# Kernel tuning notes

Measured on AMD Instinct MI355X. Metric: run time of the kernel, lower is better.

The kernel has to match this reference:

```python
import jax, jax.numpy as jnp
import numpy as np

B, N, F_IN, F, C, E = 8192, 68, 2, 128, 16, 272
EPS = 1e-15


def graph_conv(x, src, dst, W_rel, W_root, b):
    # PyG GraphConv (aggr='add'): out_i = W_rel @ sum_{j->i} x_j + W_root @ x_i + b
    agg = jnp.zeros(x.shape, x.dtype).at[:, dst].add(x[:, src])  # [B,N,Fin]
    return agg @ W_rel.T + x @ W_root.T + b


def setup_inputs() -> dict:
    key = jax.random.key(0)
    ks = jax.random.split(key, 12)
    x = jax.random.normal(ks[0], (B, N, F_IN), jnp.float32)
    edge_index = jax.random.randint(ks[1], (2, E), 0, N, jnp.int32)
    adj = jax.random.uniform(ks[2], (B, N, N), jnp.float32)
    s = jax.random.normal(ks[3], (B, N, C), jnp.float32)
    pos = jax.random.normal(ks[4], (B, N, F_IN), jnp.float32)
    sc = 0.1
    W1_rel = jax.random.normal(ks[5], (F, F_IN), jnp.float32) * sc
    W1_root = jax.random.normal(ks[6], (F, F_IN), jnp.float32) * sc
    b1 = jnp.zeros((F,), jnp.float32)
    W2_rel = jax.random.normal(ks[7], (F, F), jnp.float32) * sc
    W2_root = jax.random.normal(ks[8], (F, F), jnp.float32) * sc
    b2 = jnp.zeros((F,), jnp.float32)
    W3_rel = jax.random.normal(ks[9], (F, F), jnp.float32) * sc
    W3_root = jax.random.normal(ks[10], (F, F), jnp.float32) * sc
    b3 = jnp.zeros((F,), jnp.float32)
    return dict(x=x, edge_index=edge_index, adj=adj, s=s, pos=pos,
                W1_rel=W1_rel, W1_root=W1_root, b1=b1,
                W2_rel=W2_rel, W2_root=W2_root, b2=b2,
                W3_rel=W3_rel, W3_root=W3_root, b3=b3)


def reference(x, edge_index, adj, s, pos,
              W1_rel, W1_root, b1, W2_rel, W2_root, b2, W3_rel, W3_root, b3):
    src, dst = edge_index[0], edge_index[1]
    h = jax.nn.relu(graph_conv(x, src, dst, W1_rel, W1_root, b1))
    h = jax.nn.relu(graph_conv(h, src, dst, W2_rel, W2_root, b2))
    h = jax.nn.relu(graph_conv(h, src, dst, W3_rel, W3_root, b3))  # [B,N,F]
    # dense_diff_pool
    s_sm = jax.nn.softmax(s, axis=-1)                       # [B,N,C]
    out = jnp.einsum('bnc,bnf->bcf', s_sm, h)               # [B,C,F]
    out_adj = jnp.einsum('bnc,bnm,bmk->bck', s_sm, adj, s_sm)  # [B,C,C]
    diff = adj - jnp.einsum('bnc,bmc->bnm', s_sm, s_sm)
    link_loss = jnp.sqrt(jnp.sum(diff * diff)) / adj.size
    ent_loss = jnp.mean(jnp.sum(-s_sm * jnp.log(s_sm + EPS), axis=-1))
    return (out, out_adj, link_loss, ent_loss, pos)
```

## Files before the change

### kernel.cpp

```cpp
#include <hip/hip_runtime.h>
#include <math.h>

#define B_   8192
#define N_   68
#define FIN  2
#define F_   128
#define C_   16
#define E_   272

#define OUT_OFF  0
#define ADJ_OFF  (B_*C_*F_)
#define LINK_IDX (ADJ_OFF + B_*C_*C_)
#define ENT_IDX  (LINK_IDX + 1)
#define POS_OFF  (ENT_IDX + 1)

#define WS_CSR_OFF  131072
#define WS_W_OFF    133120
#define WS_AG_OFF   264192

typedef __attribute__((ext_vector_type(8))) short bf16x8;
typedef __attribute__((ext_vector_type(4))) float f32x4;

#define SWZ256(r, cb) (((r) * 256) + ((cb) ^ (((r) & 7) << 4)))
#define SWZ512(r, cb) (((r) * 512) + ((cb) ^ (((r) & 7) << 4)))
#define SWZH(r, cb)   (((r) * 192) + ((cb) ^ (((r) & 3) << 4)))
#define MFMA16(a, bb, c) __builtin_amdgcn_mfma_f32_16x16x32_bf16((a), (bb), (c), 0, 0, 0)

__device__ __forceinline__ short bf16_rne(float x) {
  unsigned u = __builtin_bit_cast(unsigned, x);
  u += 0x7FFFu + ((u >> 16) & 1u);
  return (short)(u >> 16);
}
__device__ __forceinline__ short4 pack4(f32x4 v) {
  short4 s;
  s.x = bf16_rne(v[0]); s.y = bf16_rne(v[1]); s.z = bf16_rne(v[2]); s.w = bf16_rne(v[3]);
  return s;
}

__global__ void prep_kernel(const int* __restrict__ edge_index,
                            const float* __restrict__ W2r, const float* __restrict__ W2o,
                            const float* __restrict__ W3r, const float* __restrict__ W3o,
                            int* __restrict__ csr, short* __restrict__ wcat,
                            short* __restrict__ agw) {
  int gid = blockIdx.x * blockDim.x + threadIdx.x;
  for (int e = gid; e < 2 * F_ * 256; e += gridDim.x * blockDim.x) {
    int layer = e >> 15, idx = e & 32767;
    int j = idx >> 8, k = idx & 255;
    const float* Wr = layer ? W3r : W2r;
    const float* Wo = layer ? W3o : W2o;
    float v = (k < F_) ? Wr[j * F_ + k] : Wo[j * F_ + (k - F_)];
    wcat[e] = bf16_rne(v);
  }
  __shared__ unsigned short cnt[80 * 128];
  __shared__ int src_s[E_], dst_s[E_], cc[N_], offs[N_ + 1];
  if (blockIdx.x == 0) {
    int t = threadIdx.x;
    for (int i = t; i < 80 * 128; i += blockDim.x) cnt[i] = 0;
    for (int e = t; e < E_; e += blockDim.x) { src_s[e] = edge_index[e]; dst_s[e] = edge_index[E_ + e]; }
    for (int n = t; n < N_; n += blockDim.x) cc[n] = 0;
    __syncthreads();
    if (t == 0) {
      for (int e = 0; e < E_; ++e) { cnt[dst_s[e] * 128 + src_s[e]]++; cc[dst_s[e]]++; }
      offs[0] = 0;
      for (int n = 0; n < N_; ++n) offs[n + 1] = offs[n] + cc[n];
      for (int n = 0; n < N_; ++n) cc[n] = offs[n];
      for (int e = 0; e < E_; ++e) { int d = dst_s[e]; csr[N_ + 1 + cc[d]++] = src_s[e]; }
      for (int n = 0; n <= N_; ++n) csr[n] = offs[n];
    }
    __syncthreads();
    for (int i = t; i < 80 * 128; i += blockDim.x) agw[i] = bf16_rne((float)cnt[i]);
  }
}

__launch_bounds__(512, 4)
__global__ void layers_kernel(
    const float* __restrict__ x, const float* __restrict__ s,
    const float* __restrict__ W1r, const float* __restrict__ W1o, const float* __restrict__ b1,
    const float* __restrict__ b2f, const float* __restrict__ b3f,
    const short* __restrict__ wcat, const short* __restrict__ agw,
    float* __restrict__ out, const int* __restrict__ csr)
{
  __shared__ __align__(16) short Hn[80 * 256];
  __shared__ __align__(16) short HT[128 * 96];
  __shared__ __align__(16) short ssmT[16 * 128];
  __shared__ float xb[N_ * FIN], axb[N_ * FIN];
  __shared__ int offs[N_ + 1], srcs[E_];

  const int b = blockIdx.x, tid = threadIdx.x;
  const int lane = tid & 63, wave = tid >> 6;
  const int l15 = lane & 15, lg = lane >> 4;
  const int j0 = wave * 16;

  for (int i = tid; i < N_ + 1; i += 512) offs[i] = csr[i];
  for (int i = tid; i < E_; i += 512) srcs[i] = csr[N_ + 1 + i];
  for (int i = tid; i < N_ * FIN; i += 512) xb[i] = x[(size_t)b * N_ * FIN + i];
  {
    int4 zz; zz.x = 0; zz.y = 0; zz.z = 0; zz.w = 0;
    for (int i = tid; i < 384; i += 512) {
      int r = 68 + (i >> 5), cb = (i & 31) * 16;
      *(int4*)((char*)Hn + SWZ512(r, cb)) = zz;
    }
    long long z8 = 0;
    for (int i = tid; i < 128 * 7; i += 512) {
      int r = i / 7, cb = 136 + (i % 7) * 8;
      *(long long*)((char*)HT + SWZH(r, cb)) = z8;
    }
    for (int i = tid; i < 16 * 7; i += 512) {
      int r = i / 7, cb = 136 + (i % 7) * 8;
      *(long long*)((char*)ssmT + SWZ256(r, cb)) = z8;
    }
  }
  if (tid < N_) {
    const float* srow = &s[((size_t)b * N_ + tid) * C_];
    float sv[16];
    float mx = -1e30f;
#pragma unroll
    for (int c = 0; c < 16; ++c) { sv[c] = srow[c]; mx = fmaxf(mx, sv[c]); }
    float sum = 0.f;
#pragma unroll
    for (int c = 0; c < 16; ++c) { sv[c] = expf(sv[c] - mx); sum += sv[c]; }
    float inv = 1.f / sum;
#pragma unroll
    for (int c = 0; c < 16; ++c)
      *(short*)((char*)ssmT + SWZ256(c, tid * 2)) = bf16_rne(sv[c] * inv);
  }
  __syncthreads();

  if (tid < N_) {
    float a0 = 0, a1 = 0;
    for (int e = offs[tid]; e < offs[tid + 1]; ++e) {
      int sr = srcs[e];
      a0 += xb[sr * 2]; a1 += xb[sr * 2 + 1];
    }
    axb[tid * 2] = a0; axb[tid * 2 + 1] = a1;
  }
  __syncthreads();

  {
    int f4 = (tid & 31) * 4;
    float4 R0 = *(const float4*)&W1r[f4 * 2], R1 = *(const float4*)&W1r[f4 * 2 + 4];
    float4 O0 = *(const float4*)&W1o[f4 * 2], O1 = *(const float4*)&W1o[f4 * 2 + 4];
    float4 Bv = *(const float4*)&b1[f4];
#pragma unroll
    for (int p = 0; p < 5; ++p) {
      int n = p * 16 + (tid >> 5);
      if (n < N_) {
        float a0 = axb[n * 2], a1 = axb[n * 2 + 1], x0 = xb[n * 2], x1 = xb[n * 2 + 1];
        f32x4 v;
        v[0] = fmaxf(a0 * R0.x + a1 * R0.y + x0 * O0.x + x1 * O0.y + Bv.x, 0.f);
        v[1] = fmaxf(a0 * R0.z + a1 * R0.w + x0 * O0.z + x1 * O0.w + Bv.y, 0.f);
        v[2] = fmaxf(a0 * R1.x + a1 * R1.y + x0 * O1.x + x1 * O1.y + Bv.z, 0.f);
        v[3] = fmaxf(a0 * R1.z + a1 * R1.w + x0 * O1.z + x1 * O1.w + Bv.w, 0.f);
        *(short4*)((char*)Hn + SWZ512(n, 256 + f4 * 2)) = pack4(v);
      }
    }
  }
  {
    int f = tid >> 2, nq = tid & 3;
    float wr0 = W1r[f * 2], wr1 = W1r[f * 2 + 1];
    float wo0 = W1o[f * 2], wo1 = W1o[f * 2 + 1];
    float bv = b1[f];
#pragma unroll
    for (int p = 0; p < 5; ++p) {
      int n0 = p * 16 + nq * 4;
      if (n0 < N_) {
        f32x4 Aa = *(const f32x4*)&axb[n0 * 2], Ab = *(const f32x4*)&axb[n0 * 2 + 4];
        f32x4 Xa = *(const f32x4*)&xb[n0 * 2],  Xb = *(const f32x4*)&xb[n0 * 2 + 4];
        f32x4 v;
        v[0] = fmaxf(Aa[0] * wr0 + Aa[1] * wr1 + Xa[0] * wo0 + Xa[1] * wo1 + bv, 0.f);
        v[1] = fmaxf(Aa[2] * wr0 + Aa[3] * wr1 + Xa[2] * wo0 + Xa[3] * wo1 + bv, 0.f);
        v[2] = fmaxf(Ab[0] * wr0 + Ab[1] * wr1 + Xb[0] * wo0 + Xb[1] * wo1 + bv, 0.f);
        v[3] = fmaxf(Ab[2] * wr0 + Ab[3] * wr1 + Xb[2] * wo0 + Xb[3] * wo1 + bv, 0.f);
        *(short4*)((char*)HT + SWZH(f, n0 * 2)) = pack4(v);
      }
    }
  }

  {
    bf16x8 hA[3];
#pragma unroll
    for (int ks = 0; ks < 3; ++ks)
      hA[ks] = *(const bf16x8*)((const char*)HT + SWZH(j0 + l15, ks * 64 + 16 * lg));
#pragma unroll
    for (int nt = 0; nt < 5; ++nt) {
      f32x4 acc = {0.f, 0.f, 0.f, 0.f};
#pragma unroll
      for (int ks = 0; ks < 3; ++ks)
        acc = MFMA16(hA[ks], *(const bf16x8*)(agw + (nt * 16 + l15) * 128 + ks * 32 + lg * 8), acc);
      *(short4*)((char*)Hn + SWZ512(nt * 16 + l15, (j0 + lg * 4) * 2)) = pack4(acc);
    }
  }
  __syncthreads();

  {
    f32x4 accL[5];
    bf16x8 Bw[8];
#pragma unroll
    for (int ks = 0; ks < 8; ++ks)
      Bw[ks] = *(const bf16x8*)(wcat + (j0 + l15) * 256 + ks * 32 + 8 * lg);
#pragma unroll
    for (int mt = 0; mt < 5; ++mt) {
      f32x4 acc = {0.f, 0.f, 0.f, 0.f};
#pragma unroll
      for (int ks = 0; ks < 8; ++ks)
        acc = MFMA16(*(const bf16x8*)((const char*)Hn + SWZ512(mt * 16 + l15, ks * 64 + 16 * lg)), Bw[ks], acc);
      accL[mt] = acc;
    }
    __syncthreads();
    float bv = b2f[j0 + l15];
#pragma unroll
    for (int mt = 0; mt < 5; ++mt) {
      f32x4 v;
#pragma unroll
      for (int r = 0; r < 4; ++r) {
        float t = accL[mt][r] + bv;
        v[r] = t > 0.f ? t : 0.f;
      }
      short4 p = pack4(v);
      *(short*)((char*)Hn + SWZ512(mt * 16 + lg * 4 + 0, 256 + (j0 + l15) * 2)) = p.x;
      *(short*)((char*)Hn + SWZ512(mt * 16 + lg * 4 + 1, 256 + (j0 + l15) * 2)) = p.y;
      *(short*)((char*)Hn + SWZ512(mt * 16 + lg * 4 + 2, 256 + (j0 + l15) * 2)) = p.z;
      *(short*)((char*)Hn + SWZ512(mt * 16 + lg * 4 + 3, 256 + (j0 + l15) * 2)) = p.w;
      *(short4*)((char*)HT + SWZH(j0 + l15, (mt * 16 + lg * 4) * 2)) = p;
    }
  }

  {
    bf16x8 hA[3];
#pragma unroll
    for (int ks = 0; ks < 3; ++ks)
      hA[ks] = *(const bf16x8*)((const char*)HT + SWZH(j0 + l15, ks * 64 + 16 * lg));
#pragma unroll
    for (int nt = 0; nt < 5; ++nt) {
      f32x4 acc = {0.f, 0.f, 0.f, 0.f};
#pragma unroll
      for (int ks = 0; ks < 3; ++ks)
        acc = MFMA16(hA[ks], *(const bf16x8*)(agw + (nt * 16 + l15) * 128 + ks * 32 + lg * 8), acc);
      *(short4*)((char*)Hn + SWZ512(nt * 16 + l15, (j0 + lg * 4) * 2)) = pack4(acc);
    }
  }
  __syncthreads();

  {
    bf16x8 Bw[8];
#pragma unroll
    for (int ks = 0; ks < 8; ++ks)
      Bw[ks] = *(const bf16x8*)(wcat + 32768 + (j0 + l15) * 256 + ks * 32 + 8 * lg);
    float bv = b3f[j0 + l15];
#pragma unroll
    for (int mt = 0; mt < 5; ++mt) {
      f32x4 acc = {0.f, 0.f, 0.f, 0.f};
#pragma unroll
      for (int ks = 0; ks < 8; ++ks)
        acc = MFMA16(*(const bf16x8*)((const char*)Hn + SWZ512(mt * 16 + l15, ks * 64 + 16 * lg)), Bw[ks], acc);
      f32x4 v;
#pragma unroll
      for (int r = 0; r < 4; ++r) {
        float t = acc[r] + bv;
        v[r] = t > 0.f ? t : 0.f;
      }
      *(short4*)((char*)HT + SWZH(j0 + l15, (mt * 16 + lg * 4) * 2)) = pack4(v);
    }
  }

  {
    f32x4 acc = {0.f, 0.f, 0.f, 0.f};
#pragma unroll
    for (int ks = 0; ks < 3; ++ks)
      acc = MFMA16(*(const bf16x8*)((const char*)HT + SWZH(j0 + l15, ks * 64 + 16 * lg)),
                   *(const bf16x8*)((const char*)ssmT + SWZ256(l15, ks * 64 + 16 * lg)), acc);
    float4 st; st.x = acc[0]; st.y = acc[1]; st.z = acc[2]; st.w = acc[3];
    *(float4*)&out[OUT_OFF + (size_t)b * C_ * F_ + l15 * F_ + j0 + lg * 4] = st;
  }
}

__launch_bounds__(512, 4)
__global__ void pool_kernel(
    const float* __restrict__ adj, const float* __restrict__ s, const float* __restrict__ pos,
    float* __restrict__ out, double* __restrict__ partials)
{
  __shared__ __align__(16) short AdjB[80 * 128];
  __shared__ __align__(16) short ssmT[16 * 128];
  __shared__ __align__(16) short TT[16 * 128];
  __shared__ double red[16];

  const int b = blockIdx.x, tid = threadIdx.x;
  const int lane = tid & 63, wave = tid >> 6;
  const int l15 = lane & 15, lg = lane >> 4;

  {
    long long z8 = 0;
    for (int i = tid; i < 1200; i += 512) {
      int r = i / 15, cb = 136 + (i % 15) * 8;
      *(long long*)((char*)AdjB + SWZ256(r, cb)) = z8;
    }
    for (int i = tid; i < 204; i += 512) {
      int r = 68 + i / 17, cb = (i % 17) * 8;
      *(long long*)((char*)AdjB + SWZ256(r, cb)) = z8;
    }
    for (int i = tid; i < 16 * 7; i += 512) {
      int r = i / 7, cb = 136 + (i % 7) * 8;
      *(long long*)((char*)ssmT + SWZ256(r, cb)) = z8;
      *(long long*)((char*)TT + SWZ256(r, cb)) = z8;
    }
  }
  float sadj2 = 0.f;
  const float* adjb = &adj[(size_t)b * N_ * N_];
  for (int q = tid; q < N_ * N_; q += 512) {
    int n = q / N_, m = q - n * N_;
    float v = adjb[q];
    sadj2 += v * v;
    *(short*)((char*)AdjB + SWZ256(n, m * 2)) = bf16_rne(v);
  }
  float entPart = 0.f;
  if (tid < N_) {
    const float* srow = &s[((size_t)b * N_ + tid) * C_];
    float sv[16], ev[16];
    float mx = -1e30f;
#pragma unroll
    for (int c = 0; c < 16; ++c) { sv[c] = srow[c]; mx = fmaxf(mx, sv[c]); }
    float sum = 0.f;
#pragma unroll
    for (int c = 0; c < 16; ++c) { ev[c] = expf(sv[c] - mx); sum += ev[c]; }
    float inv = 1.f / sum, ps = 0.f;
#pragma unroll
    for (int c = 0; c < 16; ++c) {
      float pv = ev[c] * inv;
      ps += pv * sv[c];
      *(short*)((char*)ssmT + SWZ256(c, tid * 2)) = bf16_rne(pv);
    }
    entPart = (mx + logf(sum)) - ps;
  }
  for (int i = tid; i < N_ * FIN; i += 512)
    out[POS_OFF + (size_t)b * N_ * FIN + i] = pos[(size_t)b * N_ * FIN + i];
  __syncthreads();

  float g2Part = 0.f;
  if (wave < 5) {
    f32x4 acc = {0.f, 0.f, 0.f, 0.f};
#pragma unroll
    for (int ks = 0; ks < 3; ++ks)
      acc = MFMA16(*(const bf16x8*)((const char*)AdjB + SWZ256(wave * 16 + l15, ks * 64 + 16 * lg)),
                   *(const bf16x8*)((const char*)ssmT + SWZ256(l15, ks * 64 + 16 * lg)), acc);
#pragma unroll
    for (int r = 0; r < 4; ++r) {
      int n = wave * 16 + lg * 4 + r;
      if (n < N_) *(short*)((char*)TT + SWZ256(l15, n * 2)) = bf16_rne(acc[r]);
    }
  } else if (wave == 5) {
    f32x4 acc = {0.f, 0.f, 0.f, 0.f};
#pragma unroll
    for (int ks = 0; ks < 3; ++ks) {
      bf16x8 a = *(const bf16x8*)((const char*)ssmT + SWZ256(l15, ks * 64 + 16 * lg));
      acc = MFMA16(a, a, acc);
    }
#pragma unroll
    for (int r = 0; r < 4; ++r) g2Part += acc[r] * acc[r];
  }
  __syncthreads();

  float trPart = 0.f;
  if (wave == 0) {
    f32x4 acc = {0.f, 0.f, 0.f, 0.f};
#pragma unroll
    for (int ks = 0; ks < 3; ++ks)
      acc = MFMA16(*(const bf16x8*)((const char*)ssmT + SWZ256(l15, ks * 64 + 16 * lg)),
                   *(const bf16x8*)((const char*)TT + SWZ256(l15, ks * 64 + 16 * lg)), acc);
#pragma unroll
    for (int r = 0; r < 4; ++r) {
      int c = lg * 4 + r;
      out[ADJ_OFF + (size_t)b * 256 + c * 16 + l15] = acc[r];
      if (c == l15) trPart += acc[r];
    }
  }

  double lk = (double)sadj2 - 2.0 * (double)trPart + (double)g2Part;
  double en = (double)entPart;
  for (int o = 32; o > 0; o >>= 1) { lk += __shfl_down(lk, o); en += __shfl_down(en, o); }
  if ((tid & 63) == 0) { red[wave] = lk; red[8 + wave] = en; }
  __syncthreads();
  if (tid == 0) {
    double L = 0, En = 0;
    for (int w = 0; w < 8; ++w) { L += red[w]; En += red[8 + w]; }
    partials[2 * b] = L;
    partials[2 * b + 1] = En;
  }
}

__global__ void finalize_kernel(const double* __restrict__ partials, float* __restrict__ out) {
  __shared__ double red[16];
  int tid = threadIdx.x;
  double L = 0, En = 0;
  for (int i = tid; i < B_; i += 512) { L += partials[2 * i]; En += partials[2 * i + 1]; }
  for (int o = 32; o > 0; o >>= 1) { L += __shfl_down(L, o); En += __shfl_down(En, o); }
  if ((tid & 63) == 0) { red[tid >> 6] = L; red[8 + (tid >> 6)] = En; }
  __syncthreads();
  if (tid == 0) {
    double Ls = 0, Es = 0;
    for (int w = 0; w < 8; ++w) { Ls += red[w]; Es += red[8 + w]; }
    out[LINK_IDX] = (float)(sqrt(Ls) / (double)((size_t)B_ * N_ * N_));
    out[ENT_IDX] = (float)(Es / (double)((size_t)B_ * N_));
  }
}

extern "C" void kernel_launch(void* const* d_in, const int* in_sizes, int n_in,
                              void* d_out, int out_size, void* d_ws, size_t ws_size,
                              hipStream_t stream) {
  const float* x   = (const float*)d_in[0];
  const int*   ei  = (const int*)d_in[1];
  const float* adj = (const float*)d_in[2];
  const float* s   = (const float*)d_in[3];
  const float* pos = (const float*)d_in[4];
  const float* W1r = (const float*)d_in[5];
  const float* W1o = (const float*)d_in[6];
  const float* b1  = (const float*)d_in[7];
  const float* W2r = (const float*)d_in[8];
  const float* W2o = (const float*)d_in[9];
  const float* b2  = (const float*)d_in[10];
  const float* W3r = (const float*)d_in[11];
  const float* W3o = (const float*)d_in[12];
  const float* b3  = (const float*)d_in[13];

  float* out = (float*)d_out;
  double* partials = (double*)d_ws;
  int* csr = (int*)((char*)d_ws + WS_CSR_OFF);
  short* wcat = (short*)((char*)d_ws + WS_W_OFF);
  short* agw  = (short*)((char*)d_ws + WS_AG_OFF);

  prep_kernel<<<65, 512, 0, stream>>>(ei, W2r, W2o, W3r, W3o, csr, wcat, agw);
  layers_kernel<<<B_, 512, 0, stream>>>(x, s, W1r, W1o, b1, b2, b3, wcat, agw, out, csr);
  pool_kernel<<<B_, 512, 0, stream>>>(adj, s, pos, out, partials);
  finalize_kernel<<<1, 512, 0, stream>>>(partials, out);
}
```

Before: 520.9 us.

## Retile dense layer GEMMs so each wave reuses A fragments across two column tiles

Each wave in the layer-2 and layer-3 dense GEMMs now computes two 16-column feature tiles over a subset of row tiles (3 or 2), instead of one column tile over all five row tiles. Every Hn A-fragment read from LDS then feeds two MFMAs, which roughly halves LDS reads per MFMA. In exchange the work is split unevenly between the two wave groups (3 vs 2 row tiles), each wave holds twice as many weight registers, and an extra barrier is added after layer 2's epilogue and layer 3.

```diff
diff --git a/kernel.cpp b/kernel.cpp
--- a/kernel.cpp
+++ b/kernel.cpp
@@ -72,6 +72,48 @@
   }
 }
 
+#define LG_LOAD(MI, MT) do { \
+  _Pragma("unroll") \
+  for (int ks = 0; ks < 8; ++ks) { \
+    bf16x8 a_ = *(const bf16x8*)((const char*)Hn + SWZ512((MT) * 16 + l15, ks * 64 + 16 * lg)); \
+    accA##MI = MFMA16(a_, Bw0[ks], accA##MI); \
+    accB##MI = MFMA16(a_, Bw1[ks], accB##MI); \
+  } \
+} while (0)
+
+#define EPI2(MI, MT) do { \
+  f32x4 v0_, v1_; \
+  _Pragma("unroll") \
+  for (int r = 0; r < 4; ++r) { \
+    float t0 = accA##MI[r] + bv0; v0_[r] = t0 > 0.f ? t0 : 0.f; \
+    float t1 = accB##MI[r] + bv1; v1_[r] = t1 > 0.f ? t1 : 0.f; \
+  } \
+  short4 p0_ = pack4(v0_), p1_ = pack4(v1_); \
+  int n0_ = (MT) * 16 + lg * 4; \
+  *(short*)((char*)Hn + SWZ512(n0_ + 0, 256 + f0 * 2)) = p0_.x; \
+  *(short*)((char*)Hn + SWZ512(n0_ + 1, 256 + f0 * 2)) = p0_.y; \
+  *(short*)((char*)Hn + SWZ512(n0_ + 2, 256 + f0 * 2)) = p0_.z; \
+  *(short*)((char*)Hn + SWZ512(n0_ + 3, 256 + f0 * 2)) = p0_.w; \
+  *(short*)((char*)Hn + SWZ512(n0_ + 0, 256 + f1 * 2)) = p1_.x; \
+  *(short*)((char*)Hn + SWZ512(n0_ + 1, 256 + f1 * 2)) = p1_.y; \
+  *(short*)((char*)Hn + SWZ512(n0_ + 2, 256 + f1 * 2)) = p1_.z; \
+  *(short*)((char*)Hn + SWZ512(n0_ + 3, 256 + f1 * 2)) = p1_.w; \
+  *(short4*)((char*)HT + SWZH(f0, n0_ * 2)) = p0_; \
+  *(short4*)((char*)HT + SWZH(f1, n0_ * 2)) = p1_; \
+} while (0)
+
+#define EPI3(MI, MT) do { \
+  f32x4 v0_, v1_; \
+  _Pragma("unroll") \
+  for (int r = 0; r < 4; ++r) { \
+    float t0 = accA##MI[r] + bv0; v0_[r] = t0 > 0.f ? t0 : 0.f; \
+    float t1 = accB##MI[r] + bv1; v1_[r] = t1 > 0.f ? t1 : 0.f; \
+  } \
+  int n0_ = (MT) * 16 + lg * 4; \
+  *(short4*)((char*)HT + SWZH(f0, n0_ * 2)) = pack4(v0_); \
+  *(short4*)((char*)HT + SWZH(f1, n0_ * 2)) = pack4(v1_); \
+} while (0)
+
 __launch_bounds__(512, 4)
 __global__ void layers_kernel(
     const float* __restrict__ x, const float* __restrict__ s,
@@ -90,6 +132,8 @@
   const int lane = tid & 63, wave = tid >> 6;
   const int l15 = lane & 15, lg = lane >> 4;
   const int j0 = wave * 16;
+  const int mg = wave >> 2, jg = wave & 3;
+  const int f0 = jg * 32 + l15, f1 = f0 + 16;
 
   for (int i = tid; i < N_ + 1; i += 512) offs[i] = csr[i];
   for (int i = tid; i < E_; i += 512) srcs[i] = csr[N_ + 1 + i];
@@ -177,91 +221,71 @@
   }
 
   {
-    bf16x8 hA[3];
-#pragma unroll
-    for (int ks = 0; ks < 3; ++ks)
-      hA[ks] = *(const bf16x8*)((const char*)HT + SWZH(j0 + l15, ks * 64 + 16 * lg));
+    bf16x8 hA0 = *(const bf16x8*)((const char*)HT + SWZH(j0 + l15, 0 * 64 + 16 * lg));
+    bf16x8 hA1 = *(const bf16x8*)((const char*)HT + SWZH(j0 + l15, 1 * 64 + 16 * lg));
+    bf16x8 hA2 = *(const bf16x8*)((const char*)HT + SWZH(j0 + l15, 2 * 64 + 16 * lg));
 #pragma unroll
     for (int nt = 0; nt < 5; ++nt) {
       f32x4 acc = {0.f, 0.f, 0.f, 0.f};
-#pragma unroll
-      for (int ks = 0; ks < 3; ++ks)
-        acc = MFMA16(hA[ks], *(const bf16x8*)(agw + (nt * 16 + l15) * 128 + ks * 32 + lg * 8), acc);
+      acc = MFMA16(hA0, *(const bf16x8*)(agw + (nt * 16 + l15) * 128 + 0 * 32 + lg * 8), acc);
+      acc = MFMA16(hA1, *(const bf16x8*)(agw + (nt * 16 + l15) * 128 + 1 * 32 + lg * 8), acc);
+      acc = MFMA16(hA2, *(const bf16x8*)(agw + (nt * 16 + l15) * 128 + 2 * 32 + lg * 8), acc);
       *(short4*)((char*)Hn + SWZ512(nt * 16 + l15, (j0 + lg * 4) * 2)) = pack4(acc);
     }
   }
   __syncthreads();
 
   {
-    f32x4 accL[5];
-    bf16x8 Bw[8];
-#pragma unroll
-    for (int ks = 0; ks < 8; ++ks)
-      Bw[ks] = *(const bf16x8*)(wcat + (j0 + l15) * 256 + ks * 32 + 8 * lg);
-#pragma unroll
-    for (int mt = 0; mt < 5; ++mt) {
-      f32x4 acc = {0.f, 0.f, 0.f, 0.f};
-#pragma unroll
-      for (int ks = 0; ks < 8; ++ks)
-        acc = MFMA16(*(const bf16x8*)((const char*)Hn + SWZ512(mt * 16 + l15, ks * 64 + 16 * lg)), Bw[ks], acc);
-      accL[mt] = acc;
-    }
+    bf16x8 Bw0[8], Bw1[8];
+#pragma unroll
+    for (int ks = 0; ks < 8; ++ks) {
+      Bw0[ks] = *(const bf16x8*)(wcat + f0 * 256 + ks * 32 + 8 * lg);
+      Bw1[ks] = *(const bf16x8*)(wcat + f1 * 256 + ks * 32 + 8 * lg);
+    }
+    f32x4 accA0 = {0,0,0,0}, accB0 = {0,0,0,0};
+    f32x4 accA1 = {0,0,0,0}, accB1 = {0,0,0,0};
+    f32x4 accA2 = {0,0,0,0}, accB2 = {0,0,0,0};
+    if (mg == 0) { LG_LOAD(0, 0); LG_LOAD(1, 1); LG_LOAD(2, 2); }
+    else         { LG_LOAD(0, 3); LG_LOAD(1, 4); }
     __syncthreads();
-    float bv = b2f[j0 + l15];
-#pragma unroll
-    for (int mt = 0; mt < 5; ++mt) {
-      f32x4 v;
-#pragma unroll
-      for (int r = 0; r < 4; ++r) {
-        float t = accL[mt][r] + bv;
-        v[r] = t > 0.f ? t : 0.f;
-      }
-      short4 p = pack4(v);
-      *(short*)((char*)Hn + SWZ512(mt * 16 + lg * 4 + 0, 256 + (j0 + l15) * 2)) = p.x;
-      *(short*)((char*)Hn + SWZ512(mt * 16 + lg * 4 + 1, 256 + (j0 + l15) * 2)) = p.y;
-      *(short*)((char*)Hn + SWZ512(mt * 16 + lg * 4 + 2, 256 + (j0 + l15) * 2)) = p.z;
-      *(short*)((char*)Hn + SWZ512(mt * 16 + lg * 4 + 3, 256 + (j0 + l15) * 2)) = p.w;
-      *(short4*)((char*)HT + SWZH(j0 + l15, (mt * 16 + lg * 4) * 2)) = p;
-    }
-  }
-
-  {
-    bf16x8 hA[3];
-#pragma unroll
-    for (int ks = 0; ks < 3; ++ks)
-      hA[ks] = *(const bf16x8*)((const char*)HT + SWZH(j0 + l15, ks * 64 + 16 * lg));
+    float bv0 = b2f[f0], bv1 = b2f[f1];
+    if (mg == 0) { EPI2(0, 0); EPI2(1, 1); EPI2(2, 2); }
+    else         { EPI2(0, 3); EPI2(1, 4); }
+  }
+  __syncthreads();
+
+  {
+    bf16x8 hA0 = *(const bf16x8*)((const char*)HT + SWZH(j0 + l15, 0 * 64 + 16 * lg));
+    bf16x8 hA1 = *(const bf16x8*)((const char*)HT + SWZH(j0 + l15, 1 * 64 + 16 * lg));
+    bf16x8 hA2 = *(const bf16x8*)((const char*)HT + SWZH(j0 + l15, 2 * 64 + 16 * lg));
 #pragma unroll
     for (int nt = 0; nt < 5; ++nt) {
       f32x4 acc = {0.f, 0.f, 0.f, 0.f};
-#pragma unroll
-      for (int ks = 0; ks < 3; ++ks)
-        acc = MFMA16(hA[ks], *(const bf16x8*)(agw + (nt * 16 + l15) * 128 + ks * 32 + lg * 8), acc);
+      acc = MFMA16(hA0, *(const bf16x8*)(agw + (nt * 16 + l15) * 128 + 0 * 32 + lg * 8), acc);
+      acc = MFMA16(hA1, *(const bf16x8*)(agw + (nt * 16 + l15) * 128 + 1 * 32 + lg * 8), acc);
+      acc = MFMA16(hA2, *(const bf16x8*)(agw + (nt * 16 + l15) * 128 + 2 * 32 + lg * 8), acc);
       *(short4*)((char*)Hn + SWZ512(nt * 16 + l15, (j0 + lg * 4) * 2)) = pack4(acc);
     }
   }
   __syncthreads();
 
   {
-    bf16x8 Bw[8];
-#pragma unroll
-    for (int ks = 0; ks < 8; ++ks)
-      Bw[ks] = *(const bf16x8*)(wcat + 32768 + (j0 + l15) * 256 + ks * 32 + 8 * lg);
-    float bv = b3f[j0 + l15];
-#pragma unroll
-    for (int mt = 0; mt < 5; ++mt) {
-      f32x4 acc = {0.f, 0.f, 0.f, 0.f};
-#pragma unroll
-      for (int ks = 0; ks < 8; ++ks)
-        acc = MFMA16(*(const bf16x8*)((const char*)Hn + SWZ512(mt * 16 + l15, ks * 64 + 16 * lg)), Bw[ks], acc);
-      f32x4 v;
-#pragma unroll
-      for (int r = 0; r < 4; ++r) {
-        float t = acc[r] + bv;
-        v[r] = t > 0.f ? t : 0.f;
-      }
-      *(short4*)((char*)HT + SWZH(j0 + l15, (mt * 16 + lg * 4) * 2)) = pack4(v);
-    }
-  }
+    bf16x8 Bw0[8], Bw1[8];
+#pragma unroll
+    for (int ks = 0; ks < 8; ++ks) {
+      Bw0[ks] = *(const bf16x8*)(wcat + 32768 + f0 * 256 + ks * 32 + 8 * lg);
+      Bw1[ks] = *(const bf16x8*)(wcat + 32768 + f1 * 256 + ks * 32 + 8 * lg);
+    }
+    f32x4 accA0 = {0,0,0,0}, accB0 = {0,0,0,0};
+    f32x4 accA1 = {0,0,0,0}, accB1 = {0,0,0,0};
+    f32x4 accA2 = {0,0,0,0}, accB2 = {0,0,0,0};
+    if (mg == 0) { LG_LOAD(0, 0); LG_LOAD(1, 1); LG_LOAD(2, 2); }
+    else         { LG_LOAD(0, 3); LG_LOAD(1, 4); }
+    float bv0 = b3f[f0], bv1 = b3f[f1];
+    if (mg == 0) { EPI3(0, 0); EPI3(1, 1); EPI3(2, 2); }
+    else         { EPI3(0, 3); EPI3(1, 4); }
+  }
+  __syncthreads();
 
   {
     f32x4 acc = {0.f, 0.f, 0.f, 0.f};
```

Result: slower. 661.4 us (+27.0%).

## Merge layers and pool kernels into one launch with interleaved block roles

Applied to the files above, without the earlier changes.

Replaces the separate GNN-layers and diff-pool kernels with a single kernel launched with twice as many blocks. Even blocks run the three graph-conv layers and odd blocks run the adjacency/softmax pooling and loss partials. The aim is to overlap the memory-heavy adj streaming with the MFMA-heavy layer compute on the same CUs and to drop one launch and its tail. The layer-2 MFMA loop is also reordered to interleave the five row tiles per k-step. The cost is that the union shared buffer (~72KB) is reserved for pool blocks too, which can lower their occupancy.

```diff
diff --git a/kernel.cpp b/kernel.cpp
--- a/kernel.cpp
+++ b/kernel.cpp
@@ -73,317 +73,315 @@
 }
 
 __launch_bounds__(512, 4)
-__global__ void layers_kernel(
-    const float* __restrict__ x, const float* __restrict__ s,
+__global__ void fused2_kernel(
+    const float* __restrict__ x, const float* __restrict__ adj, const float* __restrict__ s,
+    const float* __restrict__ pos,
     const float* __restrict__ W1r, const float* __restrict__ W1o, const float* __restrict__ b1,
     const float* __restrict__ b2f, const float* __restrict__ b3f,
     const short* __restrict__ wcat, const short* __restrict__ agw,
-    float* __restrict__ out, const int* __restrict__ csr)
+    float* __restrict__ out, const int* __restrict__ csr, double* __restrict__ partials)
 {
-  __shared__ __align__(16) short Hn[80 * 256];
-  __shared__ __align__(16) short HT[128 * 96];
-  __shared__ __align__(16) short ssmT[16 * 128];
-  __shared__ float xb[N_ * FIN], axb[N_ * FIN];
-  __shared__ int offs[N_ + 1], srcs[E_];
-
-  const int b = blockIdx.x, tid = threadIdx.x;
+  __shared__ __align__(16) char smem[72192];
+
+  const int bid = blockIdx.x, tid = threadIdx.x;
+  const int b = bid >> 1;
   const int lane = tid & 63, wave = tid >> 6;
   const int l15 = lane & 15, lg = lane >> 4;
-  const int j0 = wave * 16;
-
-  for (int i = tid; i < N_ + 1; i += 512) offs[i] = csr[i];
-  for (int i = tid; i < E_; i += 512) srcs[i] = csr[N_ + 1 + i];
-  for (int i = tid; i < N_ * FIN; i += 512) xb[i] = x[(size_t)b * N_ * FIN + i];
-  {
-    int4 zz; zz.x = 0; zz.y = 0; zz.z = 0; zz.w = 0;
-    for (int i = tid; i < 384; i += 512) {
-      int r = 68 + (i >> 5), cb = (i & 31) * 16;
-      *(int4*)((char*)Hn + SWZ512(r, cb)) = zz;
-    }
-    long long z8 = 0;
-    for (int i = tid; i < 128 * 7; i += 512) {
-      int r = i / 7, cb = 136 + (i % 7) * 8;
-      *(long long*)((char*)HT + SWZH(r, cb)) = z8;
-    }
-    for (int i = tid; i < 16 * 7; i += 512) {
-      int r = i / 7, cb = 136 + (i % 7) * 8;
-      *(long long*)((char*)ssmT + SWZ256(r, cb)) = z8;
-    }
-  }
-  if (tid < N_) {
-    const float* srow = &s[((size_t)b * N_ + tid) * C_];
-    float sv[16];
-    float mx = -1e30f;
-#pragma unroll
-    for (int c = 0; c < 16; ++c) { sv[c] = srow[c]; mx = fmaxf(mx, sv[c]); }
-    float sum = 0.f;
-#pragma unroll
-    for (int c = 0; c < 16; ++c) { sv[c] = expf(sv[c] - mx); sum += sv[c]; }
-    float inv = 1.f / sum;
-#pragma unroll
-    for (int c = 0; c < 16; ++c)
-      *(short*)((char*)ssmT + SWZ256(c, tid * 2)) = bf16_rne(sv[c] * inv);
-  }
-  __syncthreads();
-
-  if (tid < N_) {
-    float a0 = 0, a1 = 0;
-    for (int e = offs[tid]; e < offs[tid + 1]; ++e) {
-      int sr = srcs[e];
-      a0 += xb[sr * 2]; a1 += xb[sr * 2 + 1];
-    }
-    axb[tid * 2] = a0; axb[tid * 2 + 1] = a1;
-  }
-  __syncthreads();
-
-  {
-    int f4 = (tid & 31) * 4;
-    float4 R0 = *(const float4*)&W1r[f4 * 2], R1 = *(const float4*)&W1r[f4 * 2 + 4];
-    float4 O0 = *(const float4*)&W1o[f4 * 2], O1 = *(const float4*)&W1o[f4 * 2 + 4];
-    float4 Bv = *(const float4*)&b1[f4];
-#pragma unroll
-    for (int p = 0; p < 5; ++p) {
-      int n = p * 16 + (tid >> 5);
-      if (n < N_) {
-        float a0 = axb[n * 2], a1 = axb[n * 2 + 1], x0 = xb[n * 2], x1 = xb[n * 2 + 1];
+
+  if ((bid & 1) == 0) {
+    short* Hn   = (short*)smem;
+    short* HT   = (short*)(smem + 40960);
+    short* ssmT = (short*)(smem + 65536);
+    float* xb   = (float*)(smem + 69632);
+    float* axb  = (float*)(smem + 70176);
+    int* offs   = (int*)(smem + 70720);
+    int* srcs   = (int*)(smem + 70996);
+
+    const int j0 = wave * 16;
+
+    for (int i = tid; i < N_ + 1; i += 512) offs[i] = csr[i];
+    for (int i = tid; i < E_; i += 512) srcs[i] = csr[N_ + 1 + i];
+    for (int i = tid; i < N_ * FIN; i += 512) xb[i] = x[(size_t)b * N_ * FIN + i];
+    {
+      int4 zz; zz.x = 0; zz.y = 0; zz.z = 0; zz.w = 0;
+      for (int i = tid; i < 384; i += 512) {
+        int r = 68 + (i >> 5), cb = (i & 31) * 16;
+        *(int4*)((char*)Hn + SWZ512(r, cb)) = zz;
+      }
+      long long z8 = 0;
+      for (int i = tid; i < 128 * 7; i += 512) {
+        int r = i / 7, cb = 136 + (i % 7) * 8;
+        *(long long*)((char*)HT + SWZH(r, cb)) = z8;
+      }
+      for (int i = tid; i < 16 * 7; i += 512) {
+        int r = i / 7, cb = 136 + (i % 7) * 8;
+        *(long long*)((char*)ssmT + SWZ256(r, cb)) = z8;
+      }
+    }
+    if (tid < N_) {
+      const float* srow = &s[((size_t)b * N_ + tid) * C_];
+      float sv[16];
+      float mx = -1e30f;
+#pragma unroll
+      for (int c = 0; c < 16; ++c) { sv[c] = srow[c]; mx = fmaxf(mx, sv[c]); }
+      float sum = 0.f;
+#pragma unroll
+      for (int c = 0; c < 16; ++c) { sv[c] = expf(sv[c] - mx); sum += sv[c]; }
+      float inv = 1.f / sum;
+#pragma unroll
+      for (int c = 0; c < 16; ++c)
+        *(short*)((char*)ssmT + SWZ256(c, tid * 2)) = bf16_rne(sv[c] * inv);
+    }
+    __syncthreads();
+
+    if (tid < N_) {
+      float a0 = 0, a1 = 0;
+      for (int e = offs[tid]; e < offs[tid + 1]; ++e) {
+        int sr = srcs[e];
+        a0 += xb[sr * 2]; a1 += xb[sr * 2 + 1];
+      }
+      axb[tid * 2] = a0; axb[tid * 2 + 1] = a1;
+    }
+    __syncthreads();
+
+    {
+      int f4 = (tid & 31) * 4;
+      float4 R0 = *(const float4*)&W1r[f4 * 2], R1 = *(const float4*)&W1r[f4 * 2 + 4];
+      float4 O0 = *(const float4*)&W1o[f4 * 2], O1 = *(const float4*)&W1o[f4 * 2 + 4];
+      float4 Bv = *(const float4*)&b1[f4];
+#pragma unroll
+      for (int p = 0; p < 5; ++p) {
+        int n = p * 16 + (tid >> 5);
+        if (n < N_) {
+          float a0 = axb[n * 2], a1 = axb[n * 2 + 1], x0 = xb[n * 2], x1 = xb[n * 2 + 1];
+          f32x4 v;
+          v[0] = fmaxf(a0 * R0.x + a1 * R0.y + x0 * O0.x + x1 * O0.y + Bv.x, 0.f);
+          v[1] = fmaxf(a0 * R0.z + a1 * R0.w + x0 * O0.z + x1 * O0.w + Bv.y, 0.f);
+          v[2] = fmaxf(a0 * R1.x + a1 * R1.y + x0 * O1.x + x1 * O1.y + Bv.z, 0.f);
+          v[3] = fmaxf(a0 * R1.z + a1 * R1.w + x0 * O1.z + x1 * O1.w + Bv.w, 0.f);
+          *(short4*)((char*)Hn + SWZ512(n, 256 + f4 * 2)) = pack4(v);
+        }
+      }
+    }
+    {
+      int f = tid >> 2, nq = tid & 3;
+      float wr0 = W1r[f * 2], wr1 = W1r[f * 2 + 1];
+      float wo0 = W1o[f * 2], wo1 = W1o[f * 2 + 1];
+      float bv = b1[f];
+#pragma unroll
+      for (int p = 0; p < 5; ++p) {
+        int n0 = p * 16 + nq * 4;
+        if (n0 < N_) {
+          f32x4 Aa = *(const f32x4*)&axb[n0 * 2], Ab = *(const f32x4*)&axb[n0 * 2 + 4];
+          f32x4 Xa = *(const f32x4*)&xb[n0 * 2],  Xb = *(const f32x4*)&xb[n0 * 2 + 4];
+          f32x4 v;
+          v[0] = fmaxf(Aa[0] * wr0 + Aa[1] * wr1 + Xa[0] * wo0 + Xa[1] * wo1 + bv, 0.f);
+          v[1] = fmaxf(Aa[2] * wr0 + Aa[3] * wr1 + Xa[2] * wo0 + Xa[3] * wo1 + bv, 0.f);
+          v[2] = fmaxf(Ab[0] * wr0 + Ab[1] * wr1 + Xb[0] * wo0 + Xb[1] * wo1 + bv, 0.f);
+          v[3] = fmaxf(Ab[2] * wr0 + Ab[3] * wr1 + Xb[2] * wo0 + Xb[3] * wo1 + bv, 0.f);
+          *(short4*)((char*)HT + SWZH(f, n0 * 2)) = pack4(v);
+        }
+      }
+    }
+
+    {
+      bf16x8 hA0 = *(const bf16x8*)((const char*)HT + SWZH(j0 + l15, 0 * 64 + 16 * lg));
+      bf16x8 hA1 = *(const bf16x8*)((const char*)HT + SWZH(j0 + l15, 1 * 64 + 16 * lg));
+      bf16x8 hA2 = *(const bf16x8*)((const char*)HT + SWZH(j0 + l15, 2 * 64 + 16 * lg));
+#pragma unroll
+      for (int nt = 0; nt < 5; ++nt) {
+        f32x4 acc = {0.f, 0.f, 0.f, 0.f};
+        acc = MFMA16(hA0, *(const bf16x8*)(agw + (nt * 16 + l15) * 128 + 0 * 32 + lg * 8), acc);
+        acc = MFMA16(hA1, *(const bf16x8*)(agw + (nt * 16 + l15) * 128 + 1 * 32 + lg * 8), acc);
+        acc = MFMA16(hA2, *(const bf16x8*)(agw + (nt * 16 + l15) * 128 + 2 * 32 + lg * 8), acc);
+        *(short4*)((char*)Hn + SWZ512(nt * 16 + l15, (j0 + lg * 4) * 2)) = pack4(acc);
+      }
+    }
+    __syncthreads();
+
+    {
+      f32x4 accL0 = {0,0,0,0}, accL1 = {0,0,0,0}, accL2 = {0,0,0,0}, accL3 = {0,0,0,0}, accL4 = {0,0,0,0};
+      bf16x8 Bw[8];
+#pragma unroll
+      for (int ks = 0; ks < 8; ++ks)
+        Bw[ks] = *(const bf16x8*)(wcat + (j0 + l15) * 256 + ks * 32 + 8 * lg);
+#pragma unroll
+      for (int ks = 0; ks < 8; ++ks) {
+        accL0 = MFMA16(*(const bf16x8*)((const char*)Hn + SWZ512(0 * 16 + l15, ks * 64 + 16 * lg)), Bw[ks], accL0);
+        accL1 = MFMA16(*(const bf16x8*)((const char*)Hn + SWZ512(1 * 16 + l15, ks * 64 + 16 * lg)), Bw[ks], accL1);
+        accL2 = MFMA16(*(const bf16x8*)((const char*)Hn + SWZ512(2 * 16 + l15, ks * 64 + 16 * lg)), Bw[ks], accL2);
+        accL3 = MFMA16(*(const bf16x8*)((const char*)Hn + SWZ512(3 * 16 + l15, ks * 64 + 16 * lg)), Bw[ks], accL3);
+        accL4 = MFMA16(*(const bf16x8*)((const char*)Hn + SWZ512(4 * 16 + l15, ks * 64 + 16 * lg)), Bw[ks], accL4);
+      }
+      __syncthreads();
+      float bv = b2f[j0 + l15];
+#define EPI2_(ACC, MT) do { \
+        f32x4 v_; \
+        _Pragma("unroll") \
+        for (int r = 0; r < 4; ++r) { float t_ = ACC[r] + bv; v_[r] = t_ > 0.f ? t_ : 0.f; } \
+        short4 p_ = pack4(v_); \
+        int n0_ = (MT) * 16 + lg * 4; \
+        *(short*)((char*)Hn + SWZ512(n0_ + 0, 256 + (j0 + l15) * 2)) = p_.x; \
+        *(short*)((char*)Hn + SWZ512(n0_ + 1, 256 + (j0 + l15) * 2)) = p_.y; \
+        *(short*)((char*)Hn + SWZ512(n0_ + 2, 256 + (j0 + l15) * 2)) = p_.z; \
+        *(short*)((char*)Hn + SWZ512(n0_ + 3, 256 + (j0 + l15) * 2)) = p_.w; \
+        *(short4*)((char*)HT + SWZH(j0 + l15, n0_ * 2)) = p_; \
+      } while (0)
+      EPI2_(accL0, 0); EPI2_(accL1, 1); EPI2_(accL2, 2); EPI2_(accL3, 3); EPI2_(accL4, 4);
+#undef EPI2_
+    }
+    __syncthreads();
+
+    {
+      bf16x8 hA0 = *(const bf16x8*)((const char*)HT + SWZH(j0 + l15, 0 * 64 + 16 * lg));
+      bf16x8 hA1 = *(const bf16x8*)((const char*)HT + SWZH(j0 + l15, 1 * 64 + 16 * lg));
+      bf16x8 hA2 = *(const bf16x8*)((const char*)HT + SWZH(j0 + l15, 2 * 64 + 16 * lg));
+#pragma unroll
+      for (int nt = 0; nt < 5; ++nt) {
+        f32x4 acc = {0.f, 0.f, 0.f, 0.f};
+        acc = MFMA16(hA0, *(const bf16x8*)(agw + (nt * 16 + l15) * 128 + 0 * 32 + lg * 8), acc);
+        acc = MFMA16(hA1, *(const bf16x8*)(agw + (nt * 16 + l15) * 128 + 1 * 32 + lg * 8), acc);
+        acc = MFMA16(hA2, *(const bf16x8*)(agw + (nt * 16 + l15) * 128 + 2 * 32 + lg * 8), acc);
+        *(short4*)((char*)Hn + SWZ512(nt * 16 + l15, (j0 + lg * 4) * 2)) = pack4(acc);
+      }
+    }
+    __syncthreads();
+
+    {
+      bf16x8 Bw[8];
+#pragma unroll
+      for (int ks = 0; ks < 8; ++ks)
+        Bw[ks] = *(const bf16x8*)(wcat + 32768 + (j0 + l15) * 256 + ks * 32 + 8 * lg);
+      float bv = b3f[j0 + l15];
+#pragma unroll
+      for (int mt = 0; mt < 5; ++mt) {
+        f32x4 acc = {0.f, 0.f, 0.f, 0.f};
+#pragma unroll
+        for (int ks = 0; ks < 8; ++ks)
+          acc = MFMA16(*(const bf16x8*)((const char*)Hn + SWZ512(mt * 16 + l15, ks * 64 + 16 * lg)), Bw[ks], acc);
         f32x4 v;
-        v[0] = fmaxf(a0 * R0.x + a1 * R0.y + x0 * O0.x + x1 * O0.y + Bv.x, 0.f);
-        v[1] = fmaxf(a0 * R0.z + a1 * R0.w + x0 * O0.z + x1 * O0.w + Bv.y, 0.f);
-        v[2] = fmaxf(a0 * R1.x + a1 * R1.y + x0 * O1.x + x1 * O1.y + Bv.z, 0.f);
-        v[3] = fmaxf(a0 * R1.z + a1 * R1.w + x0 * O1.z + x1 * O1.w + Bv.w, 0.f);
-        *(short4*)((char*)Hn + SWZ512(n, 256 + f4 * 2)) = pack4(v);
-      }
-    }
-  }
-  {
-    int f = tid >> 2, nq = tid & 3;
-    float wr0 = W1r[f * 2], wr1 = W1r[f * 2 + 1];
-    float wo0 = W1o[f * 2], wo1 = W1o[f * 2 + 1];
-    float bv = b1[f];
-#pragma unroll
-    for (int p = 0; p < 5; ++p) {
-      int n0 = p * 16 + nq * 4;
-      if (n0 < N_) {
-        f32x4 Aa = *(const f32x4*)&axb[n0 * 2], Ab = *(const f32x4*)&axb[n0 * 2 + 4];
-        f32x4 Xa = *(const f32x4*)&xb[n0 * 2],  Xb = *(const f32x4*)&xb[n0 * 2 + 4];
-        f32x4 v;
-        v[0] = fmaxf(Aa[0] * wr0 + Aa[1] * wr1 + Xa[0] * wo0 + Xa[1] * wo1 + bv, 0.f);
-        v[1] = fmaxf(Aa[2] * wr0 + Aa[3] * wr1 + Xa[2] * wo0 + Xa[3] * wo1 + bv, 0.f);
-        v[2] = fmaxf(Ab[0] * wr0 + Ab[1] * wr1 + Xb[0] * wo0 + Xb[1] * wo1 + bv, 0.f);
-        v[3] = fmaxf(Ab[2] * wr0 + Ab[3] * wr1 + Xb[2] * wo0 + Xb[3] * wo1 + bv, 0.f);
-        *(short4*)((char*)HT + SWZH(f, n0 * 2)) = pack4(v);
-      }
-    }
-  }
-
-  {
-    bf16x8 hA[3];
-#pragma unroll
-    for (int ks = 0; ks < 3; ++ks)
-      hA[ks] = *(const bf16x8*)((const char*)HT + SWZH(j0 + l15, ks * 64 + 16 * lg));
-#pragma unroll
-    for (int nt = 0; nt < 5; ++nt) {
+#pragma unroll
+        for (int r = 0; r < 4; ++r) {
+          float t = acc[r] + bv;
+          v[r] = t > 0.f ? t : 0.f;
+        }
+        *(short4*)((char*)HT + SWZH(j0 + l15, (mt * 16 + lg * 4) * 2)) = pack4(v);
+      }
+    }
+
+    {
       f32x4 acc = {0.f, 0.f, 0.f, 0.f};
 #pragma unroll
       for (int ks = 0; ks < 3; ++ks)
-        acc = MFMA16(hA[ks], *(const bf16x8*)(agw + (nt * 16 + l15) * 128 + ks * 32 + lg * 8), acc);
-      *(short4*)((char*)Hn + SWZ512(nt * 16 + l15, (j0 + lg * 4) * 2)) = pack4(acc);
-    }
-  }
-  __syncthreads();
-
-  {
-    f32x4 accL[5];
-    bf16x8 Bw[8];
-#pragma unroll
-    for (int ks = 0; ks < 8; ++ks)
-      Bw[ks] = *(const bf16x8*)(wcat + (j0 + l15) * 256 + ks * 32 + 8 * lg);
-#pragma unroll
-    for (int mt = 0; mt < 5; ++mt) {
+        acc = MFMA16(*(const bf16x8*)((const char*)HT + SWZH(j0 + l15, ks * 64 + 16 * lg)),
+                     *(const bf16x8*)((const char*)ssmT + SWZ256(l15, ks * 64 + 16 * lg)), acc);
+      float4 st; st.x = acc[0]; st.y = acc[1]; st.z = acc[2]; st.w = acc[3];
+      *(float4*)&out[OUT_OFF + (size_t)b * C_ * F_ + l15 * F_ + j0 + lg * 4] = st;
+    }
+
+  } else {
+    short* AdjB  = (short*)smem;
+    short* ssmT  = (short*)(smem + 20480);
+    short* TT    = (short*)(smem + 24576);
+    double* red  = (double*)(smem + 28672);
+
+    {
+      long long z8 = 0;
+      for (int i = tid; i < 1200; i += 512) {
+        int r = i / 15, cb = 136 + (i % 15) * 8;
+        *(long long*)((char*)AdjB + SWZ256(r, cb)) = z8;
+      }
+      for (int i = tid; i < 204; i += 512) {
+        int r = 68 + i / 17, cb = (i % 17) * 8;
+        *(long long*)((char*)AdjB + SWZ256(r, cb)) = z8;
+      }
+      for (int i = tid; i < 16 * 7; i += 512) {
+        int r = i / 7, cb = 136 + (i % 7) * 8;
+        *(long long*)((char*)ssmT + SWZ256(r, cb)) = z8;
+        *(long long*)((char*)TT + SWZ256(r, cb)) = z8;
+      }
+    }
+    float sadj2 = 0.f;
+    const float* adjb = &adj[(size_t)b * N_ * N_];
+    for (int q = tid; q < N_ * N_; q += 512) {
+      int n = q / N_, m = q - n * N_;
+      float v = adjb[q];
+      sadj2 += v * v;
+      *(short*)((char*)AdjB + SWZ256(n, m * 2)) = bf16_rne(v);
+    }
+    float entPart = 0.f;
+    if (tid < N_) {
+      const float* srow = &s[((size_t)b * N_ + tid) * C_];
+      float sv[16], ev[16];
+      float mx = -1e30f;
+#pragma unroll
+      for (int c = 0; c < 16; ++c) { sv[c] = srow[c]; mx = fmaxf(mx, sv[c]); }
+      float sum = 0.f;
+#pragma unroll
+      for (int c = 0; c < 16; ++c) { ev[c] = expf(sv[c] - mx); sum += ev[c]; }
+      float inv = 1.f / sum, ps = 0.f;
+#pragma unroll
+      for (int c = 0; c < 16; ++c) {
+        float pv = ev[c] * inv;
+        ps += pv * sv[c];
+        *(short*)((char*)ssmT + SWZ256(c, tid * 2)) = bf16_rne(pv);
+      }
+      entPart = (mx + logf(sum)) - ps;
+    }
+    for (int i = tid; i < N_ * FIN; i += 512)
+      out[POS_OFF + (size_t)b * N_ * FIN + i] = pos[(size_t)b * N_ * FIN + i];
+    __syncthreads();
+
+    float g2Part = 0.f;
+    if (wave < 5) {
       f32x4 acc = {0.f, 0.f, 0.f, 0.f};
 #pragma unroll
-      for (int ks = 0; ks < 8; ++ks)
-        acc = MFMA16(*(const bf16x8*)((const char*)Hn + SWZ512(mt * 16 + l15, ks * 64 + 16 * lg)), Bw[ks], acc);
-      accL[mt] = acc;
-    }
-    __syncthreads();
-    float bv = b2f[j0 + l15];
-#pragma unroll
-    for (int mt = 0; mt < 5; ++mt) {
-      f32x4 v;
+      for (int ks = 0; ks < 3; ++ks)
+        acc = MFMA16(*(const bf16x8*)((const char*)AdjB + SWZ256(wave * 16 + l15, ks * 64 + 16 * lg)),
+                     *(const bf16x8*)((const char*)ssmT + SWZ256(l15, ks * 64 + 16 * lg)), acc);
 #pragma unroll
       for (int r = 0; r < 4; ++r) {
-        float t = accL[mt][r] + bv;
-        v[r] = t > 0.f ? t : 0.f;
-      }
-      short4 p = pack4(v);
-      *(short*)((char*)Hn + SWZ512(mt * 16 + lg * 4 + 0, 256 + (j0 + l15) * 2)) = p.x;
-      *(short*)((char*)Hn + SWZ512(mt * 16 + lg * 4 + 1, 256 + (j0 + l15) * 2)) = p.y;
-      *(short*)((char*)Hn + SWZ512(mt * 16 + lg * 4 + 2, 256 + (j0 + l15) * 2)) = p.z;
-      *(short*)((char*)Hn + SWZ512(mt * 16 + lg * 4 + 3, 256 + (j0 + l15) * 2)) = p.w;
-      *(short4*)((char*)HT + SWZH(j0 + l15, (mt * 16 + lg * 4) * 2)) = p;
-    }
-  }
-
-  {
-    bf16x8 hA[3];
-#pragma unroll
-    for (int ks = 0; ks < 3; ++ks)
-      hA[ks] = *(const bf16x8*)((const char*)HT + SWZH(j0 + l15, ks * 64 + 16 * lg));
-#pragma unroll
-    for (int nt = 0; nt < 5; ++nt) {
+        int n = wave * 16 + lg * 4 + r;
+        if (n < N_) *(short*)((char*)TT + SWZ256(l15, n * 2)) = bf16_rne(acc[r]);
+      }
+    } else if (wave == 5) {
       f32x4 acc = {0.f, 0.f, 0.f, 0.f};
 #pragma unroll
+      for (int ks = 0; ks < 3; ++ks) {
+        bf16x8 a = *(const bf16x8*)((const char*)ssmT + SWZ256(l15, ks * 64 + 16 * lg));
+        acc = MFMA16(a, a, acc);
+      }
+#pragma unroll
+      for (int r = 0; r < 4; ++r) g2Part += acc[r] * acc[r];
+    }
+    __syncthreads();
+
+    float trPart = 0.f;
+    if (wave == 0) {
+      f32x4 acc = {0.f, 0.f, 0.f, 0.f};
+#pragma unroll
       for (int ks = 0; ks < 3; ++ks)
-        acc = MFMA16(hA[ks], *(const bf16x8*)(agw + (nt * 16 + l15) * 128 + ks * 32 + lg * 8), acc);
-      *(short4*)((char*)Hn + SWZ512(nt * 16 + l15, (j0 + lg * 4) * 2)) = pack4(acc);
-    }
-  }
-  __syncthreads();
-
-  {
-    bf16x8 Bw[8];
-#pragma unroll
-    for (int ks = 0; ks < 8; ++ks)
-      Bw[ks] = *(const bf16x8*)(wcat + 32768 + (j0 + l15) * 256 + ks * 32 + 8 * lg);
-    float bv = b3f[j0 + l15];
-#pragma unroll
-    for (int mt = 0; mt < 5; ++mt) {
-      f32x4 acc = {0.f, 0.f, 0.f, 0.f};
-#pragma unroll
-      for (int ks = 0; ks < 8; ++ks)
-        acc = MFMA16(*(const bf16x8*)((const char*)Hn + SWZ512(mt * 16 + l15, ks * 64 + 16 * lg)), Bw[ks], acc);
-      f32x4 v;
+        acc = MFMA16(*(const bf16x8*)((const char*)ssmT + SWZ256(l15, ks * 64 + 16 * lg)),
+                     *(const bf16x8*)((const char*)TT + SWZ256(l15, ks * 64 + 16 * lg)), acc);
 #pragma unroll
       for (int r = 0; r < 4; ++r) {
-        float t = acc[r] + bv;
-        v[r] = t > 0.f ? t : 0.f;
-      }
-      *(short4*)((char*)HT + SWZH(j0 + l15, (mt * 16 + lg * 4) * 2)) = pack4(v);
-    }
-  }
-
-  {
-    f32x4 acc = {0.f, 0.f, 0.f, 0.f};
-#pragma unroll
-    for (int ks = 0; ks < 3; ++ks)
-      acc = MFMA16(*(const bf16x8*)((const char*)HT + SWZH(j0 + l15, ks * 64 + 16 * lg)),
-                   *(const bf16x8*)((const char*)ssmT + SWZ256(l15, ks * 64 + 16 * lg)), acc);
-    float4 st; st.x = acc[0]; st.y = acc[1]; st.z = acc[2]; st.w = acc[3];
-    *(float4*)&out[OUT_OFF + (size_t)b * C_ * F_ + l15 * F_ + j0 + lg * 4] = st;
-  }
-}
-
-__launch_bounds__(512, 4)
-__global__ void pool_kernel(
-    const float* __restrict__ adj, const float* __restrict__ s, const float* __restrict__ pos,
-    float* __restrict__ out, double* __restrict__ partials)
-{
-  __shared__ __align__(16) short AdjB[80 * 128];
-  __shared__ __align__(16) short ssmT[16 * 128];
-  __shared__ __align__(16) short TT[16 * 128];
-  __shared__ double red[16];
-
-  const int b = blockIdx.x, tid = threadIdx.x;
-  const int lane = tid & 63, wave = tid >> 6;
-  const int l15 = lane & 15, lg = lane >> 4;
-
-  {
-    long long z8 = 0;
-    for (int i = tid; i < 1200; i += 512) {
-      int r = i / 15, cb = 136 + (i % 15) * 8;
-      *(long long*)((char*)AdjB + SWZ256(r, cb)) = z8;
-    }
-    for (int i = tid; i < 204; i += 512) {
-      int r = 68 + i / 17, cb = (i % 17) * 8;
-      *(long long*)((char*)AdjB + SWZ256(r, cb)) = z8;
-    }
-    for (int i = tid; i < 16 * 7; i += 512) {
-      int r = i / 7, cb = 136 + (i % 7) * 8;
-      *(long long*)((char*)ssmT + SWZ256(r, cb)) = z8;
-      *(long long*)((char*)TT + SWZ256(r, cb)) = z8;
-    }
-  }
-  float sadj2 = 0.f;
-  const float* adjb = &adj[(size_t)b * N_ * N_];
-  for (int q = tid; q < N_ * N_; q += 512) {
-    int n = q / N_, m = q - n * N_;
-    float v = adjb[q];
-    sadj2 += v * v;
-    *(short*)((char*)AdjB + SWZ256(n, m * 2)) = bf16_rne(v);
-  }
-  float entPart = 0.f;
-  if (tid < N_) {
-    const float* srow = &s[((size_t)b * N_ + tid) * C_];
-    float sv[16], ev[16];
-    float mx = -1e30f;
-#pragma unroll
-    for (int c = 0; c < 16; ++c) { sv[c] = srow[c]; mx = fmaxf(mx, sv[c]); }
-    float sum = 0.f;
-#pragma unroll
-    for (int c = 0; c < 16; ++c) { ev[c] = expf(sv[c] - mx); sum += ev[c]; }
-    float inv = 1.f / sum, ps = 0.f;
-#pragma unroll
-    for (int c = 0; c < 16; ++c) {
-      float pv = ev[c] * inv;
-      ps += pv * sv[c];
-      *(short*)((char*)ssmT + SWZ256(c, tid * 2)) = bf16_rne(pv);
-    }
-    entPart = (mx + logf(sum)) - ps;
-  }
-  for (int i = tid; i < N_ * FIN; i += 512)
-    out[POS_OFF + (size_t)b * N_ * FIN + i] = pos[(size_t)b * N_ * FIN + i];
-  __syncthreads();
-
-  float g2Part = 0.f;
-  if (wave < 5) {
-    f32x4 acc = {0.f, 0.f, 0.f, 0.f};
-#pragma unroll
-    for (int ks = 0; ks < 3; ++ks)
-      acc = MFMA16(*(const bf16x8*)((const char*)AdjB + SWZ256(wave * 16 + l15, ks * 64 + 16 * lg)),
-                   *(const bf16x8*)((const char*)ssmT + SWZ256(l15, ks * 64 + 16 * lg)), acc);
-#pragma unroll
-    for (int r = 0; r < 4; ++r) {
-      int n = wave * 16 + lg * 4 + r;
-      if (n < N_) *(short*)((char*)TT + SWZ256(l15, n * 2)) = bf16_rne(acc[r]);
-    }
-  } else if (wave == 5) {
-    f32x4 acc = {0.f, 0.f, 0.f, 0.f};
-#pragma unroll
-    for (int ks = 0; ks < 3; ++ks) {
-      bf16x8 a = *(const bf16x8*)((const char*)ssmT + SWZ256(l15, ks * 64 + 16 * lg));
-      acc = MFMA16(a, a, acc);
-    }
-#pragma unroll
-    for (int r = 0; r < 4; ++r) g2Part += acc[r] * acc[r];
-  }
-  __syncthreads();
-
-  float trPart = 0.f;
-  if (wave == 0) {
-    f32x4 acc = {0.f, 0.f, 0.f, 0.f};
-#pragma unroll
-    for (int ks = 0; ks < 3; ++ks)
-      acc = MFMA16(*(const bf16x8*)((const char*)ssmT + SWZ256(l15, ks * 64 + 16 * lg)),
-                   *(const bf16x8*)((const char*)TT + SWZ256(l15, ks * 64 + 16 * lg)), acc);
-#pragma unroll
-    for (int r = 0; r < 4; ++r) {
-      int c = lg * 4 + r;
-      out[ADJ_OFF + (size_t)b * 256 + c * 16 + l15] = acc[r];
-      if (c == l15) trPart += acc[r];
-    }
-  }
-
-  double lk = (double)sadj2 - 2.0 * (double)trPart + (double)g2Part;
-  double en = (double)entPart;
-  for (int o = 32; o > 0; o >>= 1) { lk += __shfl_down(lk, o); en += __shfl_down(en, o); }
-  if ((tid & 63) == 0) { red[wave] = lk; red[8 + wave] = en; }
-  __syncthreads();
-  if (tid == 0) {
-    double L = 0, En = 0;
-    for (int w = 0; w < 8; ++w) { L += red[w]; En += red[8 + w]; }
-    partials[2 * b] = L;
-    partials[2 * b + 1] = En;
+        int c = lg * 4 + r;
+        out[ADJ_OFF + (size_t)b * 256 + c * 16 + l15] = acc[r];
+        if (c == l15) trPart += acc[r];
+      }
+    }
+
+    double lk = (double)sadj2 - 2.0 * (double)trPart + (double)g2Part;
+    double en = (double)entPart;
+    for (int o = 32; o > 0; o >>= 1) { lk += __shfl_down(lk, o); en += __shfl_down(en, o); }
+    if ((tid & 63) == 0) { red[wave] = lk; red[8 + wave] = en; }
+    __syncthreads();
+    if (tid == 0) {
+      double L = 0, En = 0;
+      for (int w = 0; w < 8; ++w) { L += red[w]; En += red[8 + w]; }
+      partials[2 * b] = L;
+      partials[2 * b + 1] = En;
+    }
   }
 }
 
@@ -428,7 +426,7 @@
   short* agw  = (short*)((char*)d_ws + WS_AG_OFF);
 
   prep_kernel<<<65, 512, 0, stream>>>(ei, W2r, W2o, W3r, W3o, csr, wcat, agw);
-  layers_kernel<<<B_, 512, 0, stream>>>(x, s, W1r, W1o, b1, b2, b3, wcat, agw, out, csr);
-  pool_kernel<<<B_, 512, 0, stream>>>(adj, s, pos, out, partials);
+  fused2_kernel<<<2 * B_, 512, 0, stream>>>(x, adj, s, pos, W1r, W1o, b1, b2, b3,
+                                            wcat, agw, out, csr, partials);
   finalize_kernel<<<1, 512, 0, stream>>>(partials, out);
 }
```

Result: slower. 911.9 us (+75.1%).
